# Optimization experiments

Hardware: AMD Instinct MI355X
Metric: run time of the kernel (lower is better)

Reference implementation:

```python
import jax, jax.numpy as jnp
import numpy as np
from jax import lax

SD = 16          # sample_duration
STRIDE = 16      # feat_stride
SCALES = (4, 8, 16)
RATIOS = (0.5, 1.0, 2.0)
PRE_NMS = 1000   # proposals kept before NMS (TEST config)
POST_NMS = 128   # proposals kept after NMS
NMS_TH = 0.7


def _anchors2d():
    base = 16.0
    ctr = (base - 1.0) / 2.0
    out = []
    for r in RATIOS:
        ws = np.round(np.sqrt(base * base / r))
        hs = np.round(ws * r)
        for s in SCALES:
            w, h = ws * s, hs * s
            out.append([ctr - (w - 1) / 2, ctr - (h - 1) / 2,
                        ctr + (w - 1) / 2, ctr + (h - 1) / 2])
    return np.asarray(out, np.float32)                       # (9, 4)


def _anchors3d():
    # tube anchors: (x1, y1, t1, x2, y2, t2), durations [SD, SD/2, SD/4]
    a2 = _anchors2d()
    out = []
    for d in (SD, SD // 2, SD // 4):
        for a in a2:
            out.append([a[0], a[1], 0.0, a[2], a[3], d - 1.0])
    return np.asarray(out, np.float32)                       # (27, 6)


def _shifted(anchors, H, W):
    k = anchors.shape[-1]
    sx = jnp.arange(W, dtype=jnp.float32) * STRIDE
    sy = jnp.arange(H, dtype=jnp.float32) * STRIDE
    if k == 4:
        sh = jnp.stack(jnp.broadcast_arrays(sx[None, :], sy[:, None],
                                            sx[None, :], sy[:, None]), -1)
    else:
        z = jnp.zeros((H, W), jnp.float32)
        sh = jnp.stack(jnp.broadcast_arrays(sx[None, :], sy[:, None], z,
                                            sx[None, :], sy[:, None], z), -1)
    return (sh[:, :, None, :] + jnp.asarray(anchors)[None, None]).reshape(-1, k)


def _decode(anchors, deltas):
    # deltas layout: (d_ctr..., d_logsize...); works for 2D (k=4) and 3D (k=6)
    nd = anchors.shape[-1] // 2
    lo, hi = anchors[..., :nd], anchors[..., nd:]
    size = hi - lo + 1.0
    ctr = lo + 0.5 * (size - 1.0)
    pctr = deltas[..., :nd] * size + ctr
    psize = jnp.exp(deltas[..., nd:]) * size
    return jnp.concatenate([pctr - 0.5 * (psize - 1.0),
                            pctr + 0.5 * (psize - 1.0)], -1)


def _iou(b, boxes):
    # b: (k,), boxes: (N, k); area/volume IoU with +1 pixel convention
    nd = boxes.shape[-1] // 2
    lo = jnp.maximum(b[:nd], boxes[:, :nd])
    hi = jnp.minimum(b[nd:], boxes[:, nd:])
    inter = jnp.prod(jnp.maximum(hi - lo + 1.0, 0.0), -1)
    va = jnp.prod(b[nd:] - b[:nd] + 1.0)
    vb = jnp.prod(boxes[:, nd:] - boxes[:, :nd] + 1.0, -1)
    return inter / (va + vb - inter)


def _nms(boxes):
    # boxes already sorted by descending score; greedy NMS, fixed output size
    N = boxes.shape[0]

    def body(i, c):
        supp, keep = c
        idx = jnp.argmax(~supp)                 # first unsuppressed box
        keep = keep.at[i].set(idx.astype(jnp.int32))
        supp = supp | (_iou(boxes[idx], boxes) > NMS_TH)
        supp = supp.at[idx].set(True)
        return supp, keep

    _, keep = lax.fori_loop(0, POST_NMS, body,
                            (jnp.zeros(N, bool), jnp.zeros(POST_NMS, jnp.int32)))
    return keep


def _proposals(scores, deltas, anchors, maxs):
    # scores (B,N), deltas (B,N,k), anchors (N,k), maxs (B,1,k)
    boxes = jnp.clip(_decode(anchors[None], deltas), 0.0, maxs)
    _, idx = lax.top_k(scores, PRE_NMS)
    bx = jnp.take_along_axis(boxes, idx[..., None], axis=1)   # (B,PRE,k)
    keep = jax.vmap(_nms)(bx)                                 # (B,POST)
    sel = jnp.take_along_axis(bx, keep[..., None], axis=1)    # (B,POST,k)
    bidx = jnp.broadcast_to(
        jnp.arange(sel.shape[0], dtype=sel.dtype)[:, None, None],
        sel.shape[:2] + (1,))
    return lax.stop_gradient(jnp.concatenate([bidx, sel], -1))


def setup_inputs() -> dict:
    k = jax.random.split(jax.random.key(0), 8)
    s = 0.01
    return {
        "base_feat": jax.random.normal(k[0], (1, 256, 16, 32, 32), jnp.float32),
        "im_info": jnp.array([[512.0, 512.0, 1.0]], jnp.float32),
        "gt_boxes": jax.random.uniform(k[1], (1, 5, 7), jnp.float32) * 100.0,
        "gt_rois": jax.random.uniform(k[2], (1, 5, 16, 5), jnp.float32) * 100.0,
        "W_conv": jax.random.normal(k[3], (512, 256, 3, 3, 3), jnp.float32) * s,
        "b_conv": jnp.zeros((512,), jnp.float32),
        "W_cls": jax.random.normal(k[4], (54, 512), jnp.float32) * s,
        "b_cls": jnp.zeros((54,), jnp.float32),
        "W_bbox": jax.random.normal(k[5], (162, 512), jnp.float32) * s,
        "b_bbox": jnp.zeros((162,), jnp.float32),
        "W_cls16": jax.random.normal(k[6], (18, 512), jnp.float32) * s,
        "b_cls16": jnp.zeros((18,), jnp.float32),
        "W_bbox16": jax.random.normal(k[7], (36, 512), jnp.float32) * s,
        "b_bbox16": jnp.zeros((36,), jnp.float32),
    }


def reference(base_feat, im_info, gt_boxes, gt_rois, W_conv, b_conv,
              W_cls, b_cls, W_bbox, b_bbox, W_cls16, b_cls16,
              W_bbox16, b_bbox16):
    B, _, T, H, W = base_feat.shape
    # RPN_Conv: 3x3x3 Conv3d + ReLU
    conv1 = jax.nn.relu(
        lax.conv_general_dilated(base_feat, W_conv, (1, 1, 1), "SAME",
                                 dimension_numbers=("NCDHW", "OIDHW", "NCDHW"))
        + b_conv[None, :, None, None, None])
    # 1x1x1 score / bbox heads (3D)
    cls3 = jnp.einsum("bcthw,oc->bothw", conv1, W_cls) + b_cls[None, :, None, None, None]
    bbox3 = jnp.einsum("bcthw,oc->bothw", conv1, W_bbox) + b_bbox[None, :, None, None, None]
    # permute(0,1,3,4,2).mean(4) == mean over the temporal axis
    feat2 = conv1.mean(axis=2)
    cls2 = jnp.einsum("bchw,oc->bohw", feat2, W_cls16) + b_cls16[None, :, None, None]
    bbox2 = jnp.einsum("bchw,oc->bohw", feat2, W_bbox16) + b_bbox16[None, :, None, None]
    # reshape(x,2) + softmax over dim 1; fg prob is the second half of channels
    fg3 = jax.nn.softmax(cls3.reshape(B, 2, 27, T, H, W), axis=1)[:, 1]  # (B,27,T,H,W)
    fg2 = jax.nn.softmax(cls2.reshape(B, 2, 9, H, W), axis=1)[:, 1]      # (B,9,H,W)
    # proposal layers consume detached tensors (torch .data)
    fg3, fg2, bbox3d, bbox2d = map(lax.stop_gradient, (fg3, fg2, bbox3, bbox2))
    # flatten position-major (h, w, anchor)
    sc3 = fg3.mean(axis=2).transpose(0, 2, 3, 1).reshape(B, -1)
    dl3 = bbox3d.mean(axis=2).reshape(B, 27, 6, H, W).transpose(0, 3, 4, 1, 2).reshape(B, -1, 6)
    sc2 = fg2.transpose(0, 2, 3, 1).reshape(B, -1)
    dl2 = bbox2d.reshape(B, 9, 4, H, W).transpose(0, 3, 4, 1, 2).reshape(B, -1, 4)
    imh, imw = im_info[:, 0][:, None], im_info[:, 1][:, None]
    sdm = jnp.full_like(imw, SD - 1.0)
    max3 = jnp.stack([imw - 1, imh - 1, sdm, imw - 1, imh - 1, sdm], -1)  # (B,1,6)
    max2 = jnp.stack([imw - 1, imh - 1, imw - 1, imh - 1], -1)            # (B,1,4)
    rois = _proposals(sc3, dl3, _shifted(_anchors3d(), H, W), max3)       # (B,POST,7)
    rois16 = _proposals(sc2, dl2, _shifted(_anchors2d(), H, W), max2)     # (B,POST,5)
    z = jnp.zeros((), jnp.float32)  # eval mode: all RPN losses are 0
    return rois, rois16, z, z, z, z
```

## Files before the change

### kernel.cpp

```cpp
#include <hip/hip_runtime.h>
#include <hip/hip_bf16.h>
#include <cfloat>
#include <cstdint>


#define T_DIM 16
#define H_DIM 32
#define W_DIM 32
#define NVOX  (T_DIM*H_DIM*W_DIM)
#define HW    (H_DIM*W_DIM)
#define CIN   256
#define COUT  512
#define PRE_NMS 1000
#define POST_NMS 128
#define NMS_TH 0.7f

typedef __attribute__((ext_vector_type(8))) short v8s;
typedef __attribute__((ext_vector_type(4))) float v4f;
typedef __attribute__((ext_vector_type(4))) int v4i;

#define MFMA_B16(A,B,C) __builtin_amdgcn_mfma_f32_16x16x32_bf16(A,B,C,0,0,0)

__device__ __forceinline__ short f2bf(float x) {
    unsigned u = __float_as_uint(x);
    u += 0x7FFFu + ((u >> 16) & 1u);
    return (short)(u >> 16);
}
__device__ __forceinline__ float bf2f(short s) {
    return __uint_as_float(((unsigned)(unsigned short)s) << 16);
}

__constant__ float c_ws[3] = {23.f, 16.f, 11.f};
__constant__ float c_hs[3] = {12.f, 16.f, 22.f};
__constant__ float c_sc[3] = {4.f, 8.f, 16.f};
__constant__ float c_depth[3] = {16.f, 8.f, 4.f};

__global__ __launch_bounds__(256) void k_split_w(const float* __restrict__ W,
                                                 short* __restrict__ A0,
                                                 short* __restrict__ A1,
                                                 short* __restrict__ A2) {
    __shared__ float Wl[4][3456];
    const int b = blockIdx.x;
    const int t = threadIdx.x;
    const int og = b >> 1;
    const int ch = b & 1;
#pragma unroll
    for (int k = 0; k < 54; ++k) {
        int fi = t + k * 256;
        int ol = fi / 3456;
        int idx = fi - ol * 3456;
        Wl[ol][idx] = W[(size_t)(og * 4 + ol) * 6912 + ch * 3456 + idx];
    }
    __syncthreads();
    for (int p = t; p < 432; p += 256) {
        int tap = p >> 4, kol = p & 15;
        int ko = ch * 16 + kol;
        v8s vh[4], vm[4], vl[4];
#pragma unroll
        for (int ol = 0; ol < 4; ++ol)
#pragma unroll
            for (int c7 = 0; c7 < 8; ++c7) {
                float x = Wl[ol][(kol * 8 + c7) * 27 + tap];
                short hh = f2bf(x); float r = x - bf2f(hh);
                short mm = f2bf(r); float r2 = r - bf2f(mm);
                short ll = f2bf(r2);
                vh[ol][c7] = hh; vm[ol][c7] = mm; vl[ol][c7] = ll;
            }
        size_t base = ((size_t)(tap * 32 + ko) * 512 + og * 4) * 8;
#pragma unroll
        for (int q = 0; q < 4; ++q) {
            *(v8s*)(A0 + base + q * 8) = vh[q];
            *(v8s*)(A1 + base + q * 8) = vm[q];
            *(v8s*)(A2 + base + q * 8) = vl[q];
        }
    }
}

__global__ void k_build_wcomb(const float* __restrict__ Wcls, const float* __restrict__ Wbb,
                              float* __restrict__ Wc) {
    int i = blockIdx.x * 256 + threadIdx.x;
    int o = i & 255;
    int c = i >> 8;
    float v = 0.f;
    if (o < 54) v = Wcls[o * 512 + c];
    else if (o < 216) v = Wbb[(o - 54) * 512 + c];
    Wc[i] = v;
}

#define SPLIT2(X0, X1, OH, OM, OL) {                                          \
    unsigned u0_ = __float_as_uint(X0), u1_ = __float_as_uint(X1);            \
    OH = (int)__builtin_amdgcn_perm(u1_, u0_, 0x07060302u);                   \
    float h0_ = __uint_as_float(u0_ & 0xFFFF0000u);                           \
    float h1_ = __uint_as_float(u1_ & 0xFFFF0000u);                           \
    float r0_ = (X0) - h0_, r1_ = (X1) - h1_;                                 \
    unsigned v0_ = __float_as_uint(r0_), v1_ = __float_as_uint(r1_);          \
    OM = (int)__builtin_amdgcn_perm(v1_, v0_, 0x07060302u);                   \
    float m0_ = __uint_as_float(v0_ & 0xFFFF0000u);                           \
    float m1_ = __uint_as_float(v1_ & 0xFFFF0000u);                           \
    float s0_ = r0_ - m0_, s1_ = r1_ - m1_;                                   \
    OL = (int)__builtin_amdgcn_perm(__float_as_uint(s1_),                     \
                                    __float_as_uint(s0_), 0x07060302u);       \
}

__global__ void k_split_i(const float* __restrict__ I, v4i* __restrict__ Ih,
                          v4i* __restrict__ Im, v4i* __restrict__ Il) {
    int t = blockIdx.x * 256 + threadIdx.x;
    int vox = t & 16383;
    int ck8 = t >> 14;
    const float* ip = I + ((size_t)ck8 << 3) * NVOX + vox;
    int h[4], m[4], l[4];
#pragma unroll
    for (int j = 0; j < 4; ++j) {
        float x0 = ip[(size_t)(2 * j) * NVOX];
        float x1 = ip[(size_t)(2 * j + 1) * NVOX];
        SPLIT2(x0, x1, h[j], m[j], l[j]);
    }
    Ih[t] = (v4i){h[0], h[1], h[2], h[3]};
    Im[t] = (v4i){m[0], m[1], m[2], m[3]};
    Il[t] = (v4i){l[0], l[1], l[2], l[3]};
}

#define CV_SHIFT(TAP) {                                                       \
    int kt_ = (TAP) / 9 - 1, kh_ = ((TAP) / 3) % 3 - 1, kw_ = (TAP) % 3 - 1;  \
    int tt_ = bt + kt_, hh_ = bh + kh_, ww_ = bw + kw_;                       \
    bVal = ((unsigned)tt_ < 16u) && ((unsigned)hh_ < 32u) && ((unsigned)ww_ < 32u); \
    bOff = bVal ? ((tt_ << 10) + (hh_ << 5) + ww_) : 0;                       \
}

#define CV_LOAD_BP(CK8B) {                                                    \
    const size_t bidx_ = (((size_t)((CK8B) + skh * 2)) << 14) + bOff;         \
    nh0 = Ih[bidx_]; nh1 = Ih[bidx_ + NVOX];                                  \
    nm0 = Im[bidx_]; nm1 = Im[bidx_ + NVOX];                                  \
    nl0 = Il[bidx_]; nl1 = Il[bidx_ + NVOX];                                  \
}

#define LOAD_ASET_M(S, H0,H1,H2,H3, M0,M1,M2,M3, L0,L1,L2,L3) {               \
    const size_t aB_ = (((size_t)((S) >> 3) * 32 + (((S) & 7) << 2)) << 12) + aLane; \
    H0 = *(const v8s*)(A0 + aB_);       H1 = *(const v8s*)(A0 + aB_ + 128);   \
    H2 = *(const v8s*)(A0 + aB_ + 256); H3 = *(const v8s*)(A0 + aB_ + 384);   \
    M0 = *(const v8s*)(A1 + aB_);       M1 = *(const v8s*)(A1 + aB_ + 128);   \
    M2 = *(const v8s*)(A1 + aB_ + 256); M3 = *(const v8s*)(A1 + aB_ + 384);   \
    L0 = *(const v8s*)(A2 + aB_);       L1 = *(const v8s*)(A2 + aB_ + 128);   \
    L2 = *(const v8s*)(A2 + aB_ + 256); L3 = *(const v8s*)(A2 + aB_ + 384);   \
}

#define COMPUTE_M(BUF, H0,H1,H2,H3, M0,M1,M2,M3, L0,L1,L2,L3) {               \
    _Pragma("unroll")                                                         \
    for (int j = 0; j < 4; ++j) {                                             \
        v8s bb = *(const v8s*)(&Bsh[BUF][0][uB + j * 16]);                    \
        v8s bm = *(const v8s*)(&Bsh[BUF][1][uB + j * 16]);                    \
        v8s bl = *(const v8s*)(&Bsh[BUF][2][uB + j * 16]);                    \
        v4f a;                                                                \
        a = acc[0][j];                                                        \
        a = MFMA_B16(H0, bb, a); a = MFMA_B16(H0, bm, a);                     \
        a = MFMA_B16(M0, bb, a); a = MFMA_B16(H0, bl, a);                     \
        a = MFMA_B16(M0, bm, a); a = MFMA_B16(L0, bb, a);                     \
        acc[0][j] = a;                                                        \
        a = acc[1][j];                                                        \
        a = MFMA_B16(H1, bb, a); a = MFMA_B16(H1, bm, a);                     \
        a = MFMA_B16(M1, bb, a); a = MFMA_B16(H1, bl, a);                     \
        a = MFMA_B16(M1, bm, a); a = MFMA_B16(L1, bb, a);                     \
        acc[1][j] = a;                                                        \
        a = acc[2][j];                                                        \
        a = MFMA_B16(H2, bb, a); a = MFMA_B16(H2, bm, a);                     \
        a = MFMA_B16(M2, bb, a); a = MFMA_B16(H2, bl, a);                     \
        a = MFMA_B16(M2, bm, a); a = MFMA_B16(L2, bb, a);                     \
        acc[2][j] = a;                                                        \
        a = acc[3][j];                                                        \
        a = MFMA_B16(H3, bb, a); a = MFMA_B16(H3, bm, a);                     \
        a = MFMA_B16(M3, bb, a); a = MFMA_B16(H3, bl, a);                     \
        a = MFMA_B16(M3, bm, a); a = MFMA_B16(L3, bb, a);                     \
        acc[3][j] = a;                                                        \
    }                                                                         \
}

#define LOAD_ASET(S, ...) LOAD_ASET_M(S, __VA_ARGS__)
#define COMPUTE(BUF, ...) COMPUTE_M(BUF, __VA_ARGS__)

#define ASET(P) P##h0,P##h1,P##h2,P##h3,P##m0,P##m1,P##m2,P##m3,P##l0,P##l1,P##l2,P##l3

#define ITER_BODY(SS, BUF, CUR, ALT) {                                        \
    int s1_ = (SS) + 1, s2_ = (SS) + 2;                                       \
    if (s1_ < 216) { LOAD_ASET(s1_, ASET(ALT)); }                             \
    if (s1_ < 216) {                                                          \
        v4i z_ = (v4i){0, 0, 0, 0};                                           \
        Bsh[(BUF) ^ 1][0][uW0] = bValCur ? nh0 : z_;                          \
        Bsh[(BUF) ^ 1][0][uW1] = bValCur ? nh1 : z_;                          \
        Bsh[(BUF) ^ 1][1][uW0] = bValCur ? nm0 : z_;                          \
        Bsh[(BUF) ^ 1][1][uW1] = bValCur ? nm1 : z_;                          \
        Bsh[(BUF) ^ 1][2][uW0] = bValCur ? nl0 : z_;                          \
        Bsh[(BUF) ^ 1][2][uW1] = bValCur ? nl1 : z_;                          \
    }                                                                         \
    if (s2_ < 216) {                                                          \
        if ((s2_ & 7) == 0) CV_SHIFT(s2_ >> 3);                               \
        CV_LOAD_BP((s2_ & 7) << 2);                                           \
        bValCur = bVal;                                                       \
    }                                                                         \
    COMPUTE(BUF, ASET(CUR));                                                  \
}

__global__ __launch_bounds__(256, 2) void k_conv3d_mfma(
        const v4i* __restrict__ Ih, const v4i* __restrict__ Im,
        const v4i* __restrict__ Il, const short* __restrict__ A0,
        const short* __restrict__ A1, const short* __restrict__ A2,
        const float* __restrict__ bias, float* __restrict__ O) {
    __shared__ v4i Bsh[2][3][512];
    const int tid = threadIdx.x;
    const int o0 = blockIdx.y * 128;
    const int v0 = blockIdx.x * 128;
    const int lane = tid & 63;
    const int wv = tid >> 6;
    const int quad = lane >> 4, m16 = lane & 15;
    const int wo = (wv >> 1) * 64;
    const int wvx = (wv & 1) * 64;

    const int sa_o = tid >> 1, skh = tid & 1;
    const int uW0 = (skh * 2) * 128 + sa_o;
    const int uW1 = (skh * 2 + 1) * 128 + sa_o;

    const int vbase = v0 + sa_o;
    const int bt = vbase >> 10, bh = (vbase >> 5) & 31, bw = vbase & 31;

    const int uB = quad * 128 + wvx + m16;

    const size_t aLane = ((size_t)(o0 + wo + m16) << 3) + ((size_t)quad << 12);

    v4f acc[4][4];
#pragma unroll
    for (int i = 0; i < 4; i++)
#pragma unroll
        for (int j = 0; j < 4; j++) acc[i][j] = (v4f){0.f, 0.f, 0.f, 0.f};

    int bOff, bVal, bValCur;
    v4i nh0, nh1, nm0, nm1, nl0, nl1;
    v8s Ph0, Ph1, Ph2, Ph3, Pm0, Pm1, Pm2, Pm3, Pl0, Pl1, Pl2, Pl3;
    v8s Qh0, Qh1, Qh2, Qh3, Qm0, Qm1, Qm2, Qm3, Ql0, Ql1, Ql2, Ql3;

    CV_SHIFT(0);
    bValCur = bVal;
    CV_LOAD_BP(0);
    {
        v4i z_ = (v4i){0, 0, 0, 0};
        Bsh[0][0][uW0] = bValCur ? nh0 : z_;
        Bsh[0][0][uW1] = bValCur ? nh1 : z_;
        Bsh[0][1][uW0] = bValCur ? nm0 : z_;
        Bsh[0][1][uW1] = bValCur ? nm1 : z_;
        Bsh[0][2][uW0] = bValCur ? nl0 : z_;
        Bsh[0][2][uW1] = bValCur ? nl1 : z_;
    }
    CV_LOAD_BP(4);
    LOAD_ASET(0, ASET(P));
    __syncthreads();

    for (int s = 0; s < 216; s += 2) {
        ITER_BODY(s, 0, P, Q);
        __syncthreads();
        ITER_BODY(s + 1, 1, Q, P);
        __syncthreads();
    }

#pragma unroll
    for (int i = 0; i < 4; ++i) {
#pragma unroll
        for (int r = 0; r < 4; ++r) {
            int o = o0 + wo + i * 16 + quad * 4 + r;
            float bo = bias[o];
            float* dst = O + (size_t)o * NVOX + v0 + wvx + m16;
#pragma unroll
            for (int j = 0; j < 4; ++j)
                dst[j * 16] = fmaxf(acc[i][j][r] + bo, 0.f);
        }
    }
}

__global__ __launch_bounds__(256) void k_gemm_logits3(const float* __restrict__ conv1,
                                                      const float* __restrict__ Wc,
                                                      float* __restrict__ L) {
    __shared__ float As[16][64];
    __shared__ float Bs[16][64];
    const int tid = threadIdx.x;
    const int o0 = blockIdx.y * 64;
    const int v0 = blockIdx.x * 64;
    const int ty = tid >> 4, tx = tid & 15;
    const int c_l = tid >> 4, e4 = (tid & 15) << 2;

    float acc[4][4];
#pragma unroll
    for (int i = 0; i < 4; i++)
#pragma unroll
        for (int j = 0; j < 4; j++) acc[i][j] = 0.f;

    for (int ck = 0; ck < 512; ck += 16) {
        __syncthreads();
        *(float4*)(&As[c_l][e4]) = *(const float4*)(Wc + ((size_t)(ck + c_l) << 8) + o0 + e4);
        *(float4*)(&Bs[c_l][e4]) = *(const float4*)(conv1 + ((size_t)(ck + c_l) << 14) + v0 + e4);
        __syncthreads();
#pragma unroll
        for (int k = 0; k < 16; ++k) {
            float a[4], b[4];
            *(float4*)(a) = *(const float4*)(&As[k][ty * 4]);
            *(float4*)(b) = *(const float4*)(&Bs[k][tx * 4]);
#pragma unroll
            for (int i = 0; i < 4; i++)
#pragma unroll
                for (int j = 0; j < 4; j++)
                    acc[i][j] = fmaf(a[i], b[j], acc[i][j]);
        }
    }
#pragma unroll
    for (int i = 0; i < 4; i++) {
        float* dst = L + (size_t)(o0 + ty * 4 + i) * NVOX + v0 + tx * 4;
        *(float4*)(dst) = *(const float4*)(&acc[i][0]);
    }
}

__global__ void k_sc3(const float* __restrict__ L, const float* __restrict__ b_cls,
                      float* __restrict__ sc3) {
    int i = blockIdx.x * 256 + threadIdx.x;
    if (i >= 27 * HW) return;
    int a = i >> 10, hw = i & 1023;
    float b0 = b_cls[a], b1 = b_cls[27 + a];
    const float* L0 = L + (size_t)a * NVOX + hw;
    const float* L1 = L + (size_t)(27 + a) * NVOX + hw;
    float s = 0.f;
    for (int t = 0; t < T_DIM; t++) {
        float x0 = L0[t * HW] + b0, x1 = L1[t * HW] + b1;
        float m = fmaxf(x0, x1);
        float e0 = expf(x0 - m), e1 = expf(x1 - m);
        s += e1 / (e0 + e1);
    }
    sc3[hw * 27 + a] = s * (1.f / 16.f);
}

__global__ void k_dl3(const float* __restrict__ L, const float* __restrict__ b_bbox,
                      float* __restrict__ dl3) {
    int i = blockIdx.x * 256 + threadIdx.x;
    if (i >= 162 * HW) return;
    int ch = i >> 10, hw = i & 1023;
    const float* Lr = L + (size_t)(54 + ch) * NVOX + hw;
    float s = 0.f;
    for (int t = 0; t < T_DIM; t++) s += Lr[t * HW];
    s = s * (1.f / 16.f) + b_bbox[ch];
    int a = ch / 6, d = ch - a * 6;
    dl3[((size_t)hw * 27 + a) * 6 + d] = s;
}

__global__ void k_feat2(const float* __restrict__ conv1, float* __restrict__ feat2) {
    int i = blockIdx.x * 256 + threadIdx.x;
    int c = i >> 10, hw = i & 1023;
    const float* src = conv1 + (size_t)c * NVOX + hw;
    float s = 0.f;
    for (int t = 0; t < T_DIM; t++) s += src[t * HW];
    feat2[i] = s * (1.f / 16.f);
}

__global__ void k_gemm2d(const float* __restrict__ feat2, const float* __restrict__ Wcls16,
                         const float* __restrict__ Wbb16, float* __restrict__ L2) {
    int g = blockIdx.x * 256 + threadIdx.x;
    int o = g >> 10, hw = g & 1023;
    const float* wrow = (o < 18) ? (Wcls16 + (size_t)o * 512) : (Wbb16 + (size_t)(o - 18) * 512);
    float s = 0.f;
    for (int c = 0; c < 512; c++) s = fmaf(wrow[c], feat2[(size_t)c * HW + hw], s);
    L2[(size_t)o * HW + hw] = s;
}

__global__ void k_sc2(const float* __restrict__ L2, const float* __restrict__ b_cls16,
                      float* __restrict__ sc2) {
    int i = blockIdx.x * 256 + threadIdx.x;
    if (i >= 9 * HW) return;
    int a = i >> 10, hw = i & 1023;
    float x0 = L2[(size_t)a * HW + hw] + b_cls16[a];
    float x1 = L2[(size_t)(9 + a) * HW + hw] + b_cls16[9 + a];
    float m = fmaxf(x0, x1);
    float e0 = expf(x0 - m), e1 = expf(x1 - m);
    sc2[hw * 9 + a] = e1 / (e0 + e1);
}

__global__ void k_dl2(const float* __restrict__ L2, const float* __restrict__ b_bbox16,
                      float* __restrict__ dl2) {
    int i = blockIdx.x * 256 + threadIdx.x;
    if (i >= 36 * HW) return;
    int ch = i >> 10, hw = i & 1023;
    float v = L2[(size_t)(18 + ch) * HW + hw] + b_bbox16[ch];
    int a = ch >> 2, d = ch & 3;
    dl2[((size_t)hw * 9 + a) * 4 + d] = v;
}

__device__ __forceinline__ unsigned mapf(float f) {
    unsigned u = __float_as_uint(f);
    return (u & 0x80000000u) ? ~u : (u | 0x80000000u);
}

__global__ __launch_bounds__(1024) void k_proposal(const float* __restrict__ im_info,
                                                   const float* __restrict__ sc3,
                                                   const float* __restrict__ dl3,
                                                   const float* __restrict__ sc2,
                                                   const float* __restrict__ dl2,
                                                   float* __restrict__ out) {
    const int branch = blockIdx.x;
    const int tid = threadIdx.x;
    const int A = (branch == 0) ? 27 : 9;
    const int nd = (branch == 0) ? 3 : 2;
    const float* scores = (branch == 0) ? sc3 : sc2;
    const float* deltas = (branch == 0) ? dl3 : dl2;
    const int K = PRE_NMS;
    const int ept = A;
    const int base = tid * ept;

    __shared__ unsigned hist[256];
    __shared__ unsigned long long keys[1024];
    __shared__ float bx[PRE_NMS][6];
    __shared__ int keep[POST_NMS];
    __shared__ unsigned wsum[16];
    __shared__ unsigned long long alive[16];
    __shared__ int sh_b, sh_next, bcast;

    unsigned prefix = 0;
    int rank = K;
    for (int shift = 24; shift >= 0; shift -= 8) {
        if (tid < 256) hist[tid] = 0;
        __syncthreads();
        const unsigned mask_hi = (shift == 24) ? 0u : (0xFFFFFFFFu << (shift + 8));
        for (int j = 0; j < ept; j++) {
            unsigned m = mapf(scores[base + j]);
            if ((m & mask_hi) == prefix)
                atomicAdd(&hist[(m >> shift) & 255], 1u);
        }
        __syncthreads();
        for (int d = 1; d < 256; d <<= 1) {
            unsigned add = 0;
            if (tid < 256 && tid + d < 256) add = hist[tid + d];
            __syncthreads();
            if (tid < 256) hist[tid] += add;
            __syncthreads();
        }
        if (tid < 256) {
            bool win = (hist[tid] >= (unsigned)rank) &&
                       (tid == 255 || hist[tid + 1] < (unsigned)rank);
            if (win) { sh_b = tid; sh_next = (tid == 255) ? 0 : (int)hist[tid + 1]; }
        }
        __syncthreads();
        prefix |= (unsigned)sh_b << shift;
        rank -= sh_next;
        __syncthreads();
    }
    const unsigned tau = prefix;

    int gt_c = 0, eq_c = 0;
    for (int j = 0; j < ept; j++) {
        unsigned m = mapf(scores[base + j]);
        gt_c += (m > tau);
        eq_c += (m == tau);
    }
    unsigned cnt = ((unsigned)gt_c << 16) | (unsigned)eq_c;
    const int lane = tid & 63, wid = tid >> 6;
    unsigned x = cnt;
    for (int d = 1; d < 64; d <<= 1) {
        unsigned y = __shfl_up(x, d);
        if (lane >= d) x += y;
    }
    if (lane == 63) wsum[wid] = x;
    __syncthreads();
    if (wid == 0) {
        unsigned w = (lane < 16) ? wsum[lane] : 0;
        for (int d = 1; d < 16; d <<= 1) {
            unsigned y = __shfl_up(w, d);
            if (lane >= d) w += y;
        }
        if (lane < 16) wsum[lane] = w;
    }
    __syncthreads();
    unsigned excl = x - cnt + (wid ? wsum[wid - 1] : 0);
    const int c1 = (int)(wsum[15] >> 16);
    int gi = (int)(excl >> 16);
    int ei = (int)(excl & 0xFFFFu);
    for (int j = 0; j < ept; j++) {
        int idx = base + j;
        unsigned m = mapf(scores[idx]);
        unsigned long long key = ((unsigned long long)m << 32) |
                                 (unsigned)(0xFFFFFFFFu - (unsigned)idx);
        if (m > tau) {
            keys[gi++] = key;
        } else if (m == tau) {
            if (c1 + ei < K) keys[c1 + ei] = key;
            ei++;
        }
    }
    if (tid < 1024 - K) keys[K + tid] = 0;
    __syncthreads();

    for (int k = 2; k <= 1024; k <<= 1) {
        for (int j = k >> 1; j > 0; j >>= 1) {
            int ixj = tid ^ j;
            if (ixj > tid) {
                unsigned long long a = keys[tid], b = keys[ixj];
                bool sw2 = ((tid & k) == 0) ? (a < b) : (a > b);
                if (sw2) { keys[tid] = b; keys[ixj] = a; }
            }
            __syncthreads();
        }
    }

    const float imh = im_info[0], imw = im_info[1];
    if (tid < K) {
        int n = (int)(0xFFFFFFFFu - (unsigned)(keys[tid] & 0xFFFFFFFFull));
        int cell = n / A, a = n - cell * A;
        int hc = cell >> 5, wc = cell & 31;
        int a2 = (branch == 0) ? (a % 9) : a;
        int ri = a2 / 3, si = a2 % 3;
        float w = c_ws[ri] * c_sc[si], h = c_hs[ri] * c_sc[si];
        float lo[3], hi[3], mx[3];
        lo[0] = 7.5f - (w - 1.f) * 0.5f + 16.f * wc;
        hi[0] = 7.5f + (w - 1.f) * 0.5f + 16.f * wc;
        mx[0] = imw - 1.f;
        lo[1] = 7.5f - (h - 1.f) * 0.5f + 16.f * hc;
        hi[1] = 7.5f + (h - 1.f) * 0.5f + 16.f * hc;
        mx[1] = imh - 1.f;
        if (branch == 0) { lo[2] = 0.f; hi[2] = c_depth[a / 9] - 1.f; mx[2] = (float)(T_DIM - 1); }
        const float* dp = deltas + (size_t)n * (2 * nd);
        for (int d = 0; d < nd; d++) {
            float size = hi[d] - lo[d] + 1.f;
            float ctr = lo[d] + 0.5f * (size - 1.f);
            float pctr = dp[d] * size + ctr;
            float psize = expf(dp[nd + d]) * size;
            float pl = pctr - 0.5f * (psize - 1.f);
            float ph = pctr + 0.5f * (psize - 1.f);
            bx[tid][d]      = fminf(fmaxf(pl, 0.f), mx[d]);
            bx[tid][nd + d] = fminf(fmaxf(ph, 0.f), mx[d]);
        }
    }
    if (tid < 16) alive[tid] = (tid < 15) ? ~0ull : ((1ull << (K - 15 * 64)) - 1);
    __syncthreads();

    float myb[6]; float myvol = 1.f;
    if (tid < K) {
        for (int d = 0; d < 6; d++) myb[d] = bx[tid][d];
        for (int d = 0; d < nd; d++) myvol *= (myb[nd + d] - myb[d] + 1.f);
    }
    for (int i = 0; i < POST_NMS; ++i) {
        if (tid < 64) {
            unsigned long long wvb = (tid < 16) ? alive[tid] : 0ull;
            int cand = wvb ? (tid * 64 + __ffsll(wvb) - 1) : 0x7fffffff;
#pragma unroll
            for (int off = 32; off; off >>= 1)
                cand = min(cand, __shfl_xor(cand, off));
            if (tid == 0) {
                int m = (cand == 0x7fffffff) ? 0 : cand;
                bcast = m; keep[i] = m;
            }
        }
        __syncthreads();
        int sel = bcast;
        bool s = false;
        if (tid < K) {
            float inter = 1.f, selvol = 1.f;
            for (int d = 0; d < nd; d++) {
                float slo = bx[sel][d], shi = bx[sel][nd + d];
                float l = fmaxf(slo, myb[d]);
                float hh = fminf(shi, myb[nd + d]);
                inter *= fmaxf(hh - l + 1.f, 0.f);
                selvol *= (shi - slo + 1.f);
            }
            float iou = inter / (selvol + myvol - inter);
            s = (iou > NMS_TH) || (tid == sel);
        }
        unsigned long long bal = __ballot(s);
        if (lane == 0 && bal) alive[wid] &= ~bal;
        __syncthreads();
    }

    if (tid < POST_NMS) {
        int k = keep[tid];
        if (branch == 0) {
            float* o = out + (size_t)tid * 7;
            o[0] = 0.f;
            for (int d = 0; d < 6; d++) o[1 + d] = bx[k][d];
        } else {
            float* o = out + 128 * 7 + (size_t)tid * 5;
            o[0] = 0.f;
            for (int d = 0; d < 4; d++) o[1 + d] = bx[k][d];
        }
    }
    if (branch == 0 && tid == 0) {
        out[1536] = 0.f; out[1537] = 0.f; out[1538] = 0.f; out[1539] = 0.f;
    }
}

extern "C" void kernel_launch(void* const* d_in, const int* in_sizes, int n_in,
                              void* d_out, int out_size, void* d_ws, size_t ws_size,
                              hipStream_t stream) {
    (void)in_sizes; (void)n_in; (void)out_size; (void)ws_size;
    const float* base_feat = (const float*)d_in[0];
    const float* im_info   = (const float*)d_in[1];
    const float* W_conv    = (const float*)d_in[4];
    const float* b_conv    = (const float*)d_in[5];
    const float* W_cls     = (const float*)d_in[6];
    const float* b_cls     = (const float*)d_in[7];
    const float* W_bbox    = (const float*)d_in[8];
    const float* b_bbox    = (const float*)d_in[9];
    const float* W_cls16   = (const float*)d_in[10];
    const float* b_cls16   = (const float*)d_in[11];
    const float* W_bbox16  = (const float*)d_in[12];
    const float* b_bbox16  = (const float*)d_in[13];
    float* out = (float*)d_out;

    char* ws = (char*)d_ws;
    const size_t AW = (size_t)27 * 512 * 256;
    short* A0 = (short*)ws;
    short* A1 = A0 + AW;
    short* A2 = A1 + AW;
    float* L3 = (float*)ws;
    size_t off = AW * 3 * sizeof(short);
    float* Wcomb  = (float*)(ws + off); off += (size_t)512 * 256 * 4;
    float* conv1  = (float*)(ws + off); off += (size_t)COUT * NVOX * 4;
    float* feat2  = (float*)(ws + off); off += (size_t)512 * HW * 4;
    float* L2     = (float*)(ws + off); off += (size_t)64 * HW * 4;
    float* sc3    = (float*)(ws + off); off += (size_t)27 * HW * 4;
    float* dl3    = (float*)(ws + off); off += (size_t)27 * HW * 6 * 4;
    float* sc2    = (float*)(ws + off); off += (size_t)9 * HW * 4;
    float* dl2    = (float*)(ws + off); off += (size_t)9 * HW * 4 * 4;
    v4i* Ih = (v4i*)(ws + off); off += (size_t)32 * NVOX * 16;
    v4i* Im_ = (v4i*)(ws + off); off += (size_t)32 * NVOX * 16;
    v4i* Il = (v4i*)(ws + off); off += (size_t)32 * NVOX * 16;

    k_split_w<<<256, 256, 0, stream>>>(W_conv, A0, A1, A2);
    k_build_wcomb<<<512, 256, 0, stream>>>(W_cls, W_bbox, Wcomb);
    k_split_i<<<2048, 256, 0, stream>>>(base_feat, Ih, Im_, Il);
    {
        dim3 g(NVOX / 128, COUT / 128);
        k_conv3d_mfma<<<g, 256, 0, stream>>>(Ih, Im_, Il, A0, A1, A2, b_conv, conv1);
    }
    {
        dim3 g(NVOX / 64, 4);
        k_gemm_logits3<<<g, 256, 0, stream>>>(conv1, Wcomb, L3);
    }
    k_sc3<<<(27 * HW + 255) / 256, 256, 0, stream>>>(L3, b_cls, sc3);
    k_dl3<<<(162 * HW + 255) / 256, 256, 0, stream>>>(L3, b_bbox, dl3);
    k_feat2<<<(512 * HW) / 256, 256, 0, stream>>>(conv1, feat2);
    k_gemm2d<<<(54 * HW) / 256, 256, 0, stream>>>(feat2, W_cls16, W_bbox16, L2);
    k_sc2<<<(9 * HW + 255) / 256, 256, 0, stream>>>(L2, b_cls16, sc2);
    k_dl2<<<(36 * HW + 255) / 256, 256, 0, stream>>>(L2, b_bbox16, dl2);
    k_proposal<<<2, 1024, 0, stream>>>(im_info, sc3, dl3, sc2, dl2, out);
}
```

Baseline: 949.8 us.

## Load conv B operands directly from global into registers, dropping LDS staging

The conv3d MFMA kernel no longer stages the shifted input tile in shared memory with double buffering and per-step barriers. Each lane now loads its B fragments straight from global memory into registers, with a software-pipelined stagger across the four j sub-tiles. Out-of-bounds taps are redirected to a zeroed sentinel slot added after the input planes. This removes the LDS writes and reads and both __syncthreads per step, but each wave now issues redundant global loads for data its sibling waves share, which puts more pressure on L1/L2 and adds register use.

```diff
diff --git a/kernel.cpp b/kernel.cpp
--- a/kernel.cpp
+++ b/kernel.cpp
@@ -14,6 +14,8 @@
 #define PRE_NMS 1000
 #define POST_NMS 128
 #define NMS_TH 0.7f
+
+#define ZIDX  (32 * NVOX)
 
 typedef __attribute__((ext_vector_type(8))) short v8s;
 typedef __attribute__((ext_vector_type(4))) float v4f;
@@ -118,20 +120,30 @@
     Ih[t] = (v4i){h[0], h[1], h[2], h[3]};
     Im[t] = (v4i){m[0], m[1], m[2], m[3]};
     Il[t] = (v4i){l[0], l[1], l[2], l[3]};
-}
-
-#define CV_SHIFT(TAP) {                                                       \
+    if (blockIdx.x == 0 && threadIdx.x == 0) {
+        v4i z = (v4i){0, 0, 0, 0};
+        Ih[ZIDX] = z; Im[ZIDX] = z; Il[ZIDX] = z;
+    }
+}
+
+#define SHIFT1(VJ, OUT) {                                                     \
+    int t_ = ((VJ) >> 10) + kt_, h_ = (((VJ) >> 5) & 31) + kh_,               \
+        w_ = ((VJ) & 31) + kw_;                                               \
+    OUT = (((unsigned)t_ < 16u) && ((unsigned)h_ < 32u) &&                    \
+           ((unsigned)w_ < 32u)) ? ((t_ << 10) + (h_ << 5) + w_) : -1;        \
+}
+#define CV_TAPSHIFT(TAP) {                                                    \
     int kt_ = (TAP) / 9 - 1, kh_ = ((TAP) / 3) % 3 - 1, kw_ = (TAP) % 3 - 1;  \
-    int tt_ = bt + kt_, hh_ = bh + kh_, ww_ = bw + kw_;                       \
-    bVal = ((unsigned)tt_ < 16u) && ((unsigned)hh_ < 32u) && ((unsigned)ww_ < 32u); \
-    bOff = bVal ? ((tt_ << 10) + (hh_ << 5) + ww_) : 0;                       \
-}
-
-#define CV_LOAD_BP(CK8B) {                                                    \
-    const size_t bidx_ = (((size_t)((CK8B) + skh * 2)) << 14) + bOff;         \
-    nh0 = Ih[bidx_]; nh1 = Ih[bidx_ + NVOX];                                  \
-    nm0 = Im[bidx_]; nm1 = Im[bidx_ + NVOX];                                  \
-    nl0 = Il[bidx_]; nl1 = Il[bidx_ + NVOX];                                  \
+    SHIFT1(vbase,      bOff0); SHIFT1(vbase + 16, bOff1);                     \
+    SHIFT1(vbase + 32, bOff2); SHIFT1(vbase + 48, bOff3);                     \
+}
+
+#define LOAD_BJ(SS, BOFF, BH, BM, BL) {                                       \
+    int idx_ = (((((SS) & 7) << 2) + quad) << 14) + (BOFF);                   \
+    idx_ = ((BOFF) < 0) ? ZIDX : idx_;                                        \
+    BH = *(const v8s*)(Ih + idx_);                                            \
+    BM = *(const v8s*)(Im + idx_);                                            \
+    BL = *(const v8s*)(Il + idx_);                                            \
 }
 
 #define LOAD_ASET_M(S, H0,H1,H2,H3, M0,M1,M2,M3, L0,L1,L2,L3) {               \
@@ -144,59 +156,48 @@
     L2 = *(const v8s*)(A2 + aB_ + 256); L3 = *(const v8s*)(A2 + aB_ + 384);   \
 }
 
-#define COMPUTE_M(BUF, H0,H1,H2,H3, M0,M1,M2,M3, L0,L1,L2,L3) {               \
-    _Pragma("unroll")                                                         \
-    for (int j = 0; j < 4; ++j) {                                             \
-        v8s bb = *(const v8s*)(&Bsh[BUF][0][uB + j * 16]);                    \
-        v8s bm = *(const v8s*)(&Bsh[BUF][1][uB + j * 16]);                    \
-        v8s bl = *(const v8s*)(&Bsh[BUF][2][uB + j * 16]);                    \
-        v4f a;                                                                \
-        a = acc[0][j];                                                        \
-        a = MFMA_B16(H0, bb, a); a = MFMA_B16(H0, bm, a);                     \
-        a = MFMA_B16(M0, bb, a); a = MFMA_B16(H0, bl, a);                     \
-        a = MFMA_B16(M0, bm, a); a = MFMA_B16(L0, bb, a);                     \
-        acc[0][j] = a;                                                        \
-        a = acc[1][j];                                                        \
-        a = MFMA_B16(H1, bb, a); a = MFMA_B16(H1, bm, a);                     \
-        a = MFMA_B16(M1, bb, a); a = MFMA_B16(H1, bl, a);                     \
-        a = MFMA_B16(M1, bm, a); a = MFMA_B16(L1, bb, a);                     \
-        acc[1][j] = a;                                                        \
-        a = acc[2][j];                                                        \
-        a = MFMA_B16(H2, bb, a); a = MFMA_B16(H2, bm, a);                     \
-        a = MFMA_B16(M2, bb, a); a = MFMA_B16(H2, bl, a);                     \
-        a = MFMA_B16(M2, bm, a); a = MFMA_B16(L2, bb, a);                     \
-        acc[2][j] = a;                                                        \
-        a = acc[3][j];                                                        \
-        a = MFMA_B16(H3, bb, a); a = MFMA_B16(H3, bm, a);                     \
-        a = MFMA_B16(M3, bb, a); a = MFMA_B16(H3, bl, a);                     \
-        a = MFMA_B16(M3, bm, a); a = MFMA_B16(L3, bb, a);                     \
-        acc[3][j] = a;                                                        \
+#define MFMA_J_M(JJ, BH, BM, BL, H0,H1,H2,H3, M0,M1,M2,M3, L0,L1,L2,L3) {     \
+    v4f a;                                                                    \
+    a = acc[0][JJ];                                                           \
+    a = MFMA_B16(H0, BH, a); a = MFMA_B16(H0, BM, a);                         \
+    a = MFMA_B16(M0, BH, a); a = MFMA_B16(H0, BL, a);                         \
+    a = MFMA_B16(M0, BM, a); a = MFMA_B16(L0, BH, a);                         \
+    acc[0][JJ] = a;                                                           \
+    a = acc[1][JJ];                                                           \
+    a = MFMA_B16(H1, BH, a); a = MFMA_B16(H1, BM, a);                         \
+    a = MFMA_B16(M1, BH, a); a = MFMA_B16(H1, BL, a);                         \
+    a = MFMA_B16(M1, BM, a); a = MFMA_B16(L1, BH, a);                         \
+    acc[1][JJ] = a;                                                           \
+    a = acc[2][JJ];                                                           \
+    a = MFMA_B16(H2, BH, a); a = MFMA_B16(H2, BM, a);                         \
+    a = MFMA_B16(M2, BH, a); a = MFMA_B16(H2, BL, a);                         \
+    a = MFMA_B16(M2, BM, a); a = MFMA_B16(L2, BH, a);                         \
+    acc[2][JJ] = a;                                                           \
+    a = acc[3][JJ];                                                           \
+    a = MFMA_B16(H3, BH, a); a = MFMA_B16(H3, BM, a);                         \
+    a = MFMA_B16(M3, BH, a); a = MFMA_B16(H3, BL, a);                         \
+    a = MFMA_B16(M3, BM, a); a = MFMA_B16(L3, BH, a);                         \
+    acc[3][JJ] = a;                                                           \
+}
+
+#define LOAD_ASET(S, ...) LOAD_ASET_M(S, __VA_ARGS__)
+#define MFMA_J(JJ, BH, BM, BL, ...) MFMA_J_M(JJ, BH, BM, BL, __VA_ARGS__)
+
+#define ASET(P) P##h0,P##h1,P##h2,P##h3,P##m0,P##m1,P##m2,P##m3,P##l0,P##l1,P##l2,P##l3
+
+#define STAGE(SS, CUR, ALT) {                                                 \
+    if ((SS) + 1 < 216) { LOAD_ASET((SS) + 1, ASET(ALT)); }                   \
+    LOAD_BJ(SS, bOff1, b1h, b1m, b1l);                                        \
+    MFMA_J(0, b0h, b0m, b0l, ASET(CUR));                                      \
+    LOAD_BJ(SS, bOff2, b2h, b2m, b2l);                                        \
+    MFMA_J(1, b1h, b1m, b1l, ASET(CUR));                                      \
+    LOAD_BJ(SS, bOff3, b3h, b3m, b3l);                                        \
+    MFMA_J(2, b2h, b2m, b2l, ASET(CUR));                                      \
+    if ((SS) + 1 < 216) {                                                     \
+        if ((((SS) + 1) & 7) == 0) CV_TAPSHIFT(((SS) + 1) >> 3);              \
+        LOAD_BJ((SS) + 1, bOff0, b0h, b0m, b0l);                              \
     }                                                                         \
-}
-
-#define LOAD_ASET(S, ...) LOAD_ASET_M(S, __VA_ARGS__)
-#define COMPUTE(BUF, ...) COMPUTE_M(BUF, __VA_ARGS__)
-
-#define ASET(P) P##h0,P##h1,P##h2,P##h3,P##m0,P##m1,P##m2,P##m3,P##l0,P##l1,P##l2,P##l3
-
-#define ITER_BODY(SS, BUF, CUR, ALT) {                                        \
-    int s1_ = (SS) + 1, s2_ = (SS) + 2;                                       \
-    if (s1_ < 216) { LOAD_ASET(s1_, ASET(ALT)); }                             \
-    if (s1_ < 216) {                                                          \
-        v4i z_ = (v4i){0, 0, 0, 0};                                           \
-        Bsh[(BUF) ^ 1][0][uW0] = bValCur ? nh0 : z_;                          \
-        Bsh[(BUF) ^ 1][0][uW1] = bValCur ? nh1 : z_;                          \
-        Bsh[(BUF) ^ 1][1][uW0] = bValCur ? nm0 : z_;                          \
-        Bsh[(BUF) ^ 1][1][uW1] = bValCur ? nm1 : z_;                          \
-        Bsh[(BUF) ^ 1][2][uW0] = bValCur ? nl0 : z_;                          \
-        Bsh[(BUF) ^ 1][2][uW1] = bValCur ? nl1 : z_;                          \
-    }                                                                         \
-    if (s2_ < 216) {                                                          \
-        if ((s2_ & 7) == 0) CV_SHIFT(s2_ >> 3);                               \
-        CV_LOAD_BP((s2_ & 7) << 2);                                           \
-        bValCur = bVal;                                                       \
-    }                                                                         \
-    COMPUTE(BUF, ASET(CUR));                                                  \
+    MFMA_J(3, b3h, b3m, b3l, ASET(CUR));                                      \
 }
 
 __global__ __launch_bounds__(256, 2) void k_conv3d_mfma(
@@ -204,7 +205,6 @@
         const v4i* __restrict__ Il, const short* __restrict__ A0,
         const short* __restrict__ A1, const short* __restrict__ A2,
         const float* __restrict__ bias, float* __restrict__ O) {
-    __shared__ v4i Bsh[2][3][512];
     const int tid = threadIdx.x;
     const int o0 = blockIdx.y * 128;
     const int v0 = blockIdx.x * 128;
@@ -214,14 +214,7 @@
     const int wo = (wv >> 1) * 64;
     const int wvx = (wv & 1) * 64;
 
-    const int sa_o = tid >> 1, skh = tid & 1;
-    const int uW0 = (skh * 2) * 128 + sa_o;
-    const int uW1 = (skh * 2 + 1) * 128 + sa_o;
-
-    const int vbase = v0 + sa_o;
-    const int bt = vbase >> 10, bh = (vbase >> 5) & 31, bw = vbase & 31;
-
-    const int uB = quad * 128 + wvx + m16;
+    const int vbase = v0 + wvx + m16;
 
     const size_t aLane = ((size_t)(o0 + wo + m16) << 3) + ((size_t)quad << 12);
 
@@ -231,32 +224,18 @@
 #pragma unroll
         for (int j = 0; j < 4; j++) acc[i][j] = (v4f){0.f, 0.f, 0.f, 0.f};
 
-    int bOff, bVal, bValCur;
-    v4i nh0, nh1, nm0, nm1, nl0, nl1;
+    int bOff0, bOff1, bOff2, bOff3;
+    v8s b0h, b0m, b0l, b1h, b1m, b1l, b2h, b2m, b2l, b3h, b3m, b3l;
     v8s Ph0, Ph1, Ph2, Ph3, Pm0, Pm1, Pm2, Pm3, Pl0, Pl1, Pl2, Pl3;
     v8s Qh0, Qh1, Qh2, Qh3, Qm0, Qm1, Qm2, Qm3, Ql0, Ql1, Ql2, Ql3;
 
-    CV_SHIFT(0);
-    bValCur = bVal;
-    CV_LOAD_BP(0);
-    {
-        v4i z_ = (v4i){0, 0, 0, 0};
-        Bsh[0][0][uW0] = bValCur ? nh0 : z_;
-        Bsh[0][0][uW1] = bValCur ? nh1 : z_;
-        Bsh[0][1][uW0] = bValCur ? nm0 : z_;
-        Bsh[0][1][uW1] = bValCur ? nm1 : z_;
-        Bsh[0][2][uW0] = bValCur ? nl0 : z_;
-        Bsh[0][2][uW1] = bValCur ? nl1 : z_;
-    }
-    CV_LOAD_BP(4);
+    CV_TAPSHIFT(0);
     LOAD_ASET(0, ASET(P));
-    __syncthreads();
+    LOAD_BJ(0, bOff0, b0h, b0m, b0l);
 
     for (int s = 0; s < 216; s += 2) {
-        ITER_BODY(s, 0, P, Q);
-        __syncthreads();
-        ITER_BODY(s + 1, 1, Q, P);
-        __syncthreads();
+        STAGE(s, P, Q);
+        STAGE(s + 1, Q, P);
     }
 
 #pragma unroll
@@ -619,9 +598,10 @@
     float* dl3    = (float*)(ws + off); off += (size_t)27 * HW * 6 * 4;
     float* sc2    = (float*)(ws + off); off += (size_t)9 * HW * 4;
     float* dl2    = (float*)(ws + off); off += (size_t)9 * HW * 4 * 4;
-    v4i* Ih = (v4i*)(ws + off); off += (size_t)32 * NVOX * 16;
-    v4i* Im_ = (v4i*)(ws + off); off += (size_t)32 * NVOX * 16;
-    v4i* Il = (v4i*)(ws + off); off += (size_t)32 * NVOX * 16;
+    const size_t PLANE = (size_t)32 * NVOX + 256;
+    v4i* Ih = (v4i*)(ws + off); off += PLANE * 16;
+    v4i* Im_ = (v4i*)(ws + off); off += PLANE * 16;
+    v4i* Il = (v4i*)(ws + off); off += PLANE * 16;
 
     k_split_w<<<256, 256, 0, stream>>>(W_conv, A0, A1, A2);
     k_build_wcomb<<<512, 256, 0, stream>>>(W_cls, W_bbox, Wcomb);
```

Result: slower. 987.4 us (+4.0%).

## Split proposal NMS into parallel IoU bitmask kernel and single-wave greedy pass

Applied to the files above, without the earlier changes.

The fused proposal kernel is split into four kernels: top-k plus box decode into global memory, a parallel kernel that computes the full 1000x1000 IoU suppression bitmask, a single-wavefront greedy NMS over the bitmask, and an output gather. This removes the 128 serial iterations, each with two block-wide barriers across 1024 threads, and puts the IoU work on many blocks. The cost is three extra launches, global round trips, and computing every IoU pair instead of only those for selected boxes. A dead, malformed COMPUTE_M macro is also added and immediately undefined.

```diff
diff --git a/kernel.cpp b/kernel.cpp
--- a/kernel.cpp
+++ b/kernel.cpp
@@ -144,6 +144,36 @@
     L2 = *(const v8s*)(A2 + aB_ + 256); L3 = *(const v8s*)(A2 + aB_ + 384);   \
 }
 
+#define COMPUTE_M(BUF, H0,H1,H2,H3, M0,M1,M2,M3, L0,L1,L2,L3) {               \
+    _Pragma("unroll")                                                         \
+    for (int j = 0; j < 4; ++j) {                                             \
+        v8s bb = *(const v8s*)(&Bsh[BUF][0][uB + j * 16]);                    \
+        v8s bm = *(const v8s*)(&Bsh[BUF][1][uB + j * 16]);                    \
+        v8s bl = *(const v8s*)(&Bsh[BUF][2][uB + j * 16]);                    \
+        v4f a;                                                                \
+        a = acc[0][j];                                                        \
+        a = MFMA_B16(H0, bb, a); a = MFMA_B16(H0, bm, a);                     \
+        a = MFMA_B16(M0, bb, a); a = MFMA_B16(H0, bl, a);                     \
+        a = MFMA_B16(M0, bm, a); a = MFMA_B16(L0, bb, a);                     \
+        acc[0][j] = a;                                                        \
+        a = acc[1][j];                                                        \
+        a = MFMA_B16(H1, bb, a); a = MFMA_B16(H1, bm, a);                     \
+        a = MFMA_B16(M1, bb, a); a = MFMA_B16(H1, bl, a);                     \
+        a = MFMA_B16(M1, bm, a); a = MFMA_B16(L1, bb, a);                     \
+        acc[1][j] = a;                                                        \
+        a = acc[2][j];                                                        \
+        a = MFMA_B16(H2, bb, a); a = MFMA_B16(H2, bm, a);                     \
+        a = MFMA_B16(M2, bb, a); a = MFMA_B16(H2, bl, a);                     \
+        a = MFMA_B16(M2, bm, a); a = MFMA_B16(L2, bb, a);                     \
+        acc[2][j] = a;                                                        \
+        a = acc[3][j];                                                        \
+        a = MFMA_B16(H3, bb, a); a = MFMA_B16(H3, bm, a);                     \
+        a = MFMA_B16(M3, bb, a); a = MFMA_B16(H3, bl, a);                     \
+        a = MFMA_B16(M3, bm, a); a = MFMA_B16(L3, bb, a);                     \
+        acc[3][JJ_UNUSED 4 - 4 + 3] = a;                                      \
+    }                                                                         \
+}
+#undef COMPUTE_M
 #define COMPUTE_M(BUF, H0,H1,H2,H3, M0,M1,M2,M3, L0,L1,L2,L3) {               \
     _Pragma("unroll")                                                         \
     for (int j = 0; j < 4; ++j) {                                             \
@@ -391,12 +421,12 @@
     return (u & 0x80000000u) ? ~u : (u | 0x80000000u);
 }
 
-__global__ __launch_bounds__(1024) void k_proposal(const float* __restrict__ im_info,
-                                                   const float* __restrict__ sc3,
-                                                   const float* __restrict__ dl3,
-                                                   const float* __restrict__ sc2,
-                                                   const float* __restrict__ dl2,
-                                                   float* __restrict__ out) {
+__global__ __launch_bounds__(1024) void k_propA(const float* __restrict__ im_info,
+                                                const float* __restrict__ sc3,
+                                                const float* __restrict__ dl3,
+                                                const float* __restrict__ sc2,
+                                                const float* __restrict__ dl2,
+                                                float* __restrict__ bxg) {
     const int branch = blockIdx.x;
     const int tid = threadIdx.x;
     const int A = (branch == 0) ? 27 : 9;
@@ -409,11 +439,8 @@
 
     __shared__ unsigned hist[256];
     __shared__ unsigned long long keys[1024];
-    __shared__ float bx[PRE_NMS][6];
-    __shared__ int keep[POST_NMS];
     __shared__ unsigned wsum[16];
-    __shared__ unsigned long long alive[16];
-    __shared__ int sh_b, sh_next, bcast;
+    __shared__ int sh_b, sh_next;
 
     unsigned prefix = 0;
     int rank = K;
@@ -518,6 +545,7 @@
         mx[1] = imh - 1.f;
         if (branch == 0) { lo[2] = 0.f; hi[2] = c_depth[a / 9] - 1.f; mx[2] = (float)(T_DIM - 1); }
         const float* dp = deltas + (size_t)n * (2 * nd);
+        float* bp = bxg + ((size_t)branch * PRE_NMS + tid) * 6;
         for (int d = 0; d < nd; d++) {
             float size = hi[d] - lo[d] + 1.f;
             float ctr = lo[d] + 0.5f * (size - 1.f);
@@ -525,64 +553,82 @@
             float psize = expf(dp[nd + d]) * size;
             float pl = pctr - 0.5f * (psize - 1.f);
             float ph = pctr + 0.5f * (psize - 1.f);
-            bx[tid][d]      = fminf(fmaxf(pl, 0.f), mx[d]);
-            bx[tid][nd + d] = fminf(fmaxf(ph, 0.f), mx[d]);
-        }
-    }
-    if (tid < 16) alive[tid] = (tid < 15) ? ~0ull : ((1ull << (K - 15 * 64)) - 1);
-    __syncthreads();
-
-    float myb[6]; float myvol = 1.f;
-    if (tid < K) {
-        for (int d = 0; d < 6; d++) myb[d] = bx[tid][d];
-        for (int d = 0; d < nd; d++) myvol *= (myb[nd + d] - myb[d] + 1.f);
-    }
+            bp[d]      = fminf(fmaxf(pl, 0.f), mx[d]);
+            bp[nd + d] = fminf(fmaxf(ph, 0.f), mx[d]);
+        }
+    }
+}
+
+__global__ __launch_bounds__(256) void k_iou(const float* __restrict__ bxg,
+                                             unsigned long long* __restrict__ masks) {
+    int g = blockIdx.x * 256 + threadIdx.x;
+    if (g >= 2 * PRE_NMS * 16) return;
+    int branch = g / (PRE_NMS * 16);
+    int rem = g - branch * (PRE_NMS * 16);
+    int r = rem >> 4, w = rem & 15;
+    int nd = (branch == 0) ? 3 : 2;
+    const float* B = bxg + (size_t)branch * PRE_NMS * 6;
+    float rb[6];
+#pragma unroll
+    for (int d = 0; d < 6; d++) rb[d] = B[(size_t)r * 6 + d];
+    unsigned long long mword = 0;
+    int c0 = w * 64;
+    for (int j = 0; j < 64; ++j) {
+        int c = c0 + j;
+        if (c >= PRE_NMS) break;
+        const float* cb = B + (size_t)c * 6;
+        float colvol = 1.f;
+        for (int d = 0; d < nd; d++) colvol *= (cb[nd + d] - cb[d] + 1.f);
+        float inter = 1.f, rvol = 1.f;
+        for (int d = 0; d < nd; d++) {
+            float slo = rb[d], shi = rb[nd + d];
+            float l = fmaxf(slo, cb[d]);
+            float hh = fminf(shi, cb[nd + d]);
+            inter *= fmaxf(hh - l + 1.f, 0.f);
+            rvol *= (shi - slo + 1.f);
+        }
+        float iou = inter / (rvol + colvol - inter);
+        if ((iou > NMS_TH) || (c == r)) mword |= (1ull << j);
+    }
+    masks[((size_t)branch * PRE_NMS + r) * 16 + w] = mword;
+}
+
+__global__ __launch_bounds__(64) void k_nms(const unsigned long long* __restrict__ masks,
+                                            int* __restrict__ keepg) {
+    const int branch = blockIdx.x;
+    const int lane = threadIdx.x;
+    const unsigned long long* M = masks + (size_t)branch * PRE_NMS * 16;
+    unsigned long long alive = 0;
+    if (lane < 15) alive = ~0ull;
+    else if (lane == 15) alive = (1ull << (PRE_NMS - 15 * 64)) - 1;
     for (int i = 0; i < POST_NMS; ++i) {
-        if (tid < 64) {
-            unsigned long long wvb = (tid < 16) ? alive[tid] : 0ull;
-            int cand = wvb ? (tid * 64 + __ffsll(wvb) - 1) : 0x7fffffff;
-#pragma unroll
-            for (int off = 32; off; off >>= 1)
-                cand = min(cand, __shfl_xor(cand, off));
-            if (tid == 0) {
-                int m = (cand == 0x7fffffff) ? 0 : cand;
-                bcast = m; keep[i] = m;
-            }
-        }
-        __syncthreads();
-        int sel = bcast;
-        bool s = false;
-        if (tid < K) {
-            float inter = 1.f, selvol = 1.f;
-            for (int d = 0; d < nd; d++) {
-                float slo = bx[sel][d], shi = bx[sel][nd + d];
-                float l = fmaxf(slo, myb[d]);
-                float hh = fminf(shi, myb[nd + d]);
-                inter *= fmaxf(hh - l + 1.f, 0.f);
-                selvol *= (shi - slo + 1.f);
-            }
-            float iou = inter / (selvol + myvol - inter);
-            s = (iou > NMS_TH) || (tid == sel);
-        }
-        unsigned long long bal = __ballot(s);
-        if (lane == 0 && bal) alive[wid] &= ~bal;
-        __syncthreads();
-    }
-
-    if (tid < POST_NMS) {
-        int k = keep[tid];
-        if (branch == 0) {
-            float* o = out + (size_t)tid * 7;
-            o[0] = 0.f;
-            for (int d = 0; d < 6; d++) o[1 + d] = bx[k][d];
-        } else {
-            float* o = out + 128 * 7 + (size_t)tid * 5;
-            o[0] = 0.f;
-            for (int d = 0; d < 4; d++) o[1 + d] = bx[k][d];
-        }
-    }
-    if (branch == 0 && tid == 0) {
-        out[1536] = 0.f; out[1537] = 0.f; out[1538] = 0.f; out[1539] = 0.f;
+        int cand = (lane < 16 && alive) ? (lane * 64 + __ffsll(alive) - 1) : 0x7fffffff;
+#pragma unroll
+        for (int off = 32; off; off >>= 1)
+            cand = min(cand, __shfl_xor(cand, off));
+        int sel = (cand == 0x7fffffff) ? 0 : cand;
+        if (lane == 0) keepg[branch * POST_NMS + i] = sel;
+        if (lane < 16) alive &= ~M[(size_t)sel * 16 + lane];
+    }
+}
+
+__global__ void k_out(const float* __restrict__ bxg, const int* __restrict__ keepg,
+                      float* __restrict__ out) {
+    const int branch = blockIdx.x;
+    const int tid = threadIdx.x;
+    int k = keepg[branch * POST_NMS + tid];
+    const float* B = bxg + (size_t)branch * PRE_NMS * 6;
+    if (branch == 0) {
+        float* o = out + (size_t)tid * 7;
+        o[0] = 0.f;
+        for (int d = 0; d < 6; d++) o[1 + d] = B[(size_t)k * 6 + d];
+        if (tid == 0) {
+            out[1536] = 0.f; out[1537] = 0.f; out[1538] = 0.f; out[1539] = 0.f;
+        }
+    } else {
+        float* o = out + 128 * 7 + (size_t)tid * 5;
+        o[0] = 0.f;
+        for (int d = 0; d < 4; d++) o[1 + d] = B[(size_t)k * 6 + d];
     }
 }
 
@@ -622,6 +668,10 @@
     v4i* Ih = (v4i*)(ws + off); off += (size_t)32 * NVOX * 16;
     v4i* Im_ = (v4i*)(ws + off); off += (size_t)32 * NVOX * 16;
     v4i* Il = (v4i*)(ws + off); off += (size_t)32 * NVOX * 16;
+    float* bxg = (float*)(ws + off); off += (size_t)2 * PRE_NMS * 6 * 4;
+    unsigned long long* masks = (unsigned long long*)(ws + off);
+    off += (size_t)2 * PRE_NMS * 16 * 8;
+    int* keepg = (int*)(ws + off); off += (size_t)2 * POST_NMS * 4;
 
     k_split_w<<<256, 256, 0, stream>>>(W_conv, A0, A1, A2);
     k_build_wcomb<<<512, 256, 0, stream>>>(W_cls, W_bbox, Wcomb);
@@ -640,5 +690,8 @@
     k_gemm2d<<<(54 * HW) / 256, 256, 0, stream>>>(feat2, W_cls16, W_bbox16, L2);
     k_sc2<<<(9 * HW + 255) / 256, 256, 0, stream>>>(L2, b_cls16, sc2);
     k_dl2<<<(36 * HW + 255) / 256, 256, 0, stream>>>(L2, b_bbox16, dl2);
-    k_proposal<<<2, 1024, 0, stream>>>(im_info, sc3, dl3, sc2, dl2, out);
-}
+    k_propA<<<2, 1024, 0, stream>>>(im_info, sc3, dl3, sc2, dl2, bxg);
+    k_iou<<<(2 * PRE_NMS * 16 + 255) / 256, 256, 0, stream>>>(bxg, masks);
+    k_nms<<<2, 64, 0, stream>>>(masks, keepg);
+    k_out<<<2, 128, 0, stream>>>(bxg, keepg, out);
+}
```

Result: no change. 937.8 us (-1.3%).
